# Performance work log

Hardware: AMD Instinct MI355X
Metric: run time of the kernel (lower is better)

Reference implementation:

```python
import jax, jax.numpy as jnp
import numpy as np

NPOINT = 1024
RADIUS = 0.2
NSAMPLE = 32


def furthest_point_sampling(xyz, npoint):
    # xyz: (B, N, 3) -> (B, npoint) int32 indices
    B, N, _ = xyz.shape

    def step(carry, _):
        dist, far = carry
        centroid = jnp.take_along_axis(xyz, far[:, None, None], axis=1)  # (B,1,3)
        d = jnp.sum((xyz - centroid) ** 2, axis=-1)                       # (B,N)
        dist = jnp.minimum(dist, d)
        new_far = jnp.argmax(dist, axis=-1).astype(jnp.int32)
        return (dist, new_far), far

    init = (jnp.full((B, N), 1e10, xyz.dtype), jnp.zeros((B,), jnp.int32))
    _, idx = jax.lax.scan(step, init, None, length=npoint)
    return idx.T  # (B, npoint)


def ball_query(xyz, new_xyz, radius, nsample):
    # xyz: (B,N,3), new_xyz: (B,S,3) -> (B,S,nsample) int32 indices
    N = xyz.shape[1]
    d2 = jnp.sum((new_xyz[:, :, None, :] - xyz[:, None, :, :]) ** 2, axis=-1)  # (B,S,N)
    # pick first `nsample` indices within radius (CUDA ball_query semantics)
    key = jnp.where(d2 < radius * radius, jnp.arange(N, dtype=jnp.int32)[None, None, :], N)
    idx = jnp.sort(key, axis=-1)[..., :nsample]          # (B,S,nsample)
    first = idx[..., :1]
    idx = jnp.where(idx == N, first, idx)                # pad with first valid
    return jnp.clip(idx, 0, N - 1).astype(jnp.int32)     # guard empty balls


def sa_forward(xyz, features, W1, s1, b1, W2, s2, b2, W3, s3, b3):
    B, N, _ = xyz.shape
    center_idx = furthest_point_sampling(xyz, NPOINT)                     # (B,S)
    new_xyz = jnp.take_along_axis(xyz, center_idx[..., None], axis=1)     # (B,S,3)

    idx = ball_query(xyz, new_xyz, RADIUS, NSAMPLE)                       # (B,S,K)
    # group xyz (relative coords) and features
    g_xyz = jnp.take_along_axis(xyz[:, None], idx[..., None], axis=2)     # (B,S,K,3)
    g_xyz = g_xyz - new_xyz[:, :, None, :]
    feats_n = jnp.swapaxes(features, 1, 2)                                # (B,N,C)
    g_feat = jnp.take_along_axis(feats_n[:, None], idx[..., None], axis=2)  # (B,S,K,C)
    g = jnp.concatenate([g_xyz, g_feat], axis=-1)                         # (B,S,K,3+C)
    x = jnp.transpose(g, (0, 3, 1, 2))                                    # (B,3+C,S,K)

    # 1x1 conv MLP with (folded) BN affine + ReLU
    for W, s, b in ((W1, s1, b1), (W2, s2, b2), (W3, s3, b3)):
        x = jax.nn.relu(jnp.einsum('oi,bisk->bosk', W, x)
                        * s[None, :, None, None] + b[None, :, None, None])
    new_features = jnp.max(x, axis=-1)                                    # (B,Cout,S)
    return new_xyz, new_features


def setup_inputs() -> dict:
    key = jax.random.key(0)
    ks = jax.random.split(key, 11)
    B, N, C = 4, 16384, 64
    return {
        'xyz': jax.random.uniform(ks[0], (B, N, 3), jnp.float32),
        'features': jax.random.normal(ks[1], (B, C, N), jnp.float32),
        'W1': jax.random.normal(ks[2], (64, C + 3), jnp.float32) * 0.1,
        's1': jax.random.uniform(ks[3], (64,), jnp.float32),
        'b1': jax.random.normal(ks[4], (64,), jnp.float32) * 0.1,
        'W2': jax.random.normal(ks[5], (64, 64), jnp.float32) * 0.1,
        's2': jax.random.uniform(ks[6], (64,), jnp.float32),
        'b2': jax.random.normal(ks[7], (64,), jnp.float32) * 0.1,
        'W3': jax.random.normal(ks[8], (128, 64), jnp.float32) * 0.1,
        's3': jax.random.uniform(ks[9], (128,), jnp.float32),
        'b3': jax.random.normal(ks[10], (128,), jnp.float32) * 0.1,
    }


def reference(xyz, features, W1, s1, b1, W2, s2, b2, W3, s3, b3):
    return sa_forward(xyz, features, W1, s1, b1, W2, s2, b2, W3, s3, b3)
```

## Files before the change

### kernel.cpp

```cpp
#include <hip/hip_runtime.h>
#include <cstdint>
#include <cstddef>

#define BATCH   4
#define NPTS    16384
#define NPOINT  1024
#define NSAMPLE 32
#define CIN     67
#define R2f     0.04f

#define FPS_T   512
#define FPS_P   32

template <int CTRL, int RMASK>
__device__ __forceinline__ void amax_dpp(float& v, int& i) {
  int nv = __builtin_amdgcn_update_dpp(__float_as_int(v), __float_as_int(v),
                                       CTRL, RMASK, 0xf, false);
  int ni = __builtin_amdgcn_update_dpp(i, i, CTRL, RMASK, 0xf, false);
  float fv = __int_as_float(nv);
  bool tk = (fv > v) || (fv == v && ni < i);
  v = tk ? fv : v;
  i = tk ? ni : i;
}

__global__ __launch_bounds__(FPS_T, 2) void fps_kernel(
    const float* __restrict__ xyz, float* __restrict__ out_newxyz)
{
  const int b = blockIdx.x;
  const float* base = xyz + (size_t)b * NPTS * 3;
  const int t = threadIdx.x;
  const int lane = t & 63, w = t >> 6;

  float px[FPS_P], py[FPS_P], pz[FPS_P], dist[FPS_P];
#pragma unroll
  for (int j = 0; j < FPS_P; ++j) {
    int p = t + (j << 9);
    px[j] = base[p * 3 + 0];
    py[j] = base[p * 3 + 1];
    pz[j] = base[p * 3 + 2];
    dist[j] = 1e10f;
  }

  __shared__ float s_wv[2][8];
  __shared__ int   s_wi[2][8];

  float cx = base[0], cy = base[1], cz = base[2];

  for (int it = 0; it < NPOINT; ++it) {
    if (t == 0) {
      int o = (b * NPOINT + it) * 3;
      out_newxyz[o + 0] = cx;
      out_newxyz[o + 1] = cy;
      out_newxyz[o + 2] = cz;
    }
    float bv = -1.0f; int bi = 0x7fffffff;
#pragma unroll
    for (int j = 0; j < FPS_P; ++j) {
      float dx = __fsub_rn(px[j], cx);
      float dy = __fsub_rn(py[j], cy);
      float dz = __fsub_rn(pz[j], cz);
      float d  = __fadd_rn(__fadd_rn(__fmul_rn(dx, dx), __fmul_rn(dy, dy)),
                           __fmul_rn(dz, dz));
      float nd = fminf(dist[j], d);
      dist[j] = nd;
      bool tk = nd > bv;
      bv = tk ? nd : bv;
      bi = tk ? (t + (j << 9)) : bi;
    }
    amax_dpp<0x121, 0xf>(bv, bi);
    amax_dpp<0x122, 0xf>(bv, bi);
    amax_dpp<0x124, 0xf>(bv, bi);
    amax_dpp<0x128, 0xf>(bv, bi);
    amax_dpp<0x142, 0xa>(bv, bi);
    amax_dpp<0x143, 0xc>(bv, bi);

    const int par = it & 1;
    if (lane == 63) { s_wv[par][w] = bv; s_wi[par][w] = bi; }
    __syncthreads();

    float gv = s_wv[par][lane & 7];
    int   gi = s_wi[par][lane & 7];
    amax_dpp<0x121, 0xf>(gv, gi);
    amax_dpp<0x122, 0xf>(gv, gi);
    amax_dpp<0x124, 0xf>(gv, gi);

    int far = __builtin_amdgcn_readfirstlane(gi);
    cx = base[far * 3 + 0];
    cy = base[far * 3 + 1];
    cz = base[far * 3 + 2];
  }
}

__global__ __launch_bounds__(256) void transpose_kernel(
    const float* __restrict__ f, float* __restrict__ ft)
{
  __shared__ float tile[64][65];
  int b  = blockIdx.x >> 8;
  int n0 = (blockIdx.x & 255) << 6;
  for (int v = threadIdx.x; v < 64 * 64; v += 256) {
    int c = v >> 6, j = v & 63;
    tile[c][j] = f[((size_t)(b * 64 + c)) * NPTS + n0 + j];
  }
  __syncthreads();
  for (int v = threadIdx.x; v < 64 * 64; v += 256) {
    int j = v >> 6, c = v & 63;
    ft[((size_t)(b * NPTS + n0 + j)) * 64 + c] = tile[c][j];
  }
}

__global__ __launch_bounds__(1024) void mlp_kernel(
    const float* __restrict__ xyz,
    const float* __restrict__ feats,
    const float* __restrict__ featsT,
    const float* __restrict__ nx,
    const float* __restrict__ W1, const float* __restrict__ s1, const float* __restrict__ b1,
    const float* __restrict__ W2, const float* __restrict__ s2, const float* __restrict__ b2,
    const float* __restrict__ W3, const float* __restrict__ s3, const float* __restrict__ b3,
    float* __restrict__ outF)
{
  __shared__ float W1t[CIN * 64];
  __shared__ float W2t[64 * 64];
  __shared__ float sb[512];
  __shared__ float xs[CIN * 34];
  __shared__ float h1[64 * 34];
  __shared__ float h2[64 * 34];
  __shared__ int   hm[128];
  __shared__ int   lid8[8][NSAMPLE];

  const int tid = threadIdx.x;
  const int lane = tid & 63, w = tid >> 6;

  for (int v = tid; v < CIN * 64; v += 1024) {
    int o = v / CIN, i = v - o * CIN;
    W1t[i * 64 + o] = W1[v];
  }
  for (int v = tid; v < 64 * 64; v += 1024) {
    int o = v >> 6, i = v & 63;
    W2t[i * 64 + o] = W2[v];
  }
  if (tid < 64)       sb[tid]       = s1[tid];
  else if (tid < 128) sb[tid]       = b1[tid - 64];
  else if (tid < 192) sb[tid]       = s2[tid - 128];
  else if (tid < 256) sb[tid]       = b2[tid - 192];
  else if (tid < 384) sb[tid]       = s3[tid - 256];
  else if (tid < 512) sb[tid]       = b3[tid - 384];

  if (w < 8) {
    int g = (blockIdx.x << 3) + w;
    int b = g >> 10;
    const float* base = xyz + (size_t)b * NPTS * 3;
    float cx = nx[g * 3 + 0], cy = nx[g * 3 + 1], cz = nx[g * 3 + 2];
    int cnt = 0, fidx = -1;
    for (int c0 = 0; c0 < NPTS && cnt < NSAMPLE; c0 += 64) {
      int i = c0 + lane;
      float dx = __fsub_rn(base[i * 3 + 0], cx);
      float dy = __fsub_rn(base[i * 3 + 1], cy);
      float dz = __fsub_rn(base[i * 3 + 2], cz);
      float d2 = __fadd_rn(__fadd_rn(__fmul_rn(dx, dx), __fmul_rn(dy, dy)),
                           __fmul_rn(dz, dz));
      bool pred = d2 < R2f;
      unsigned long long mk = __ballot(pred);
      if (pred) {
        int rank = cnt + __popcll(mk & ((1ull << lane) - 1ull));
        if (rank < NSAMPLE) lid8[w][rank] = i;
        if (rank == 0) fidx = i;
      }
      cnt += __popcll(mk);
    }
#pragma unroll
    for (int off = 32; off >= 1; off >>= 1) {
      int o = __shfl_xor(fidx, off);
      fidx = o > fidx ? o : fidx;
    }
    if (lane >= cnt && lane < NSAMPLE) lid8[w][lane] = fidx;
  }
  __syncthreads();

  for (int ci = 0; ci < 8; ++ci) {
    int g = (blockIdx.x << 3) + ci;
    int b = g >> 10, m = g & 1023;

    {
      int k = tid >> 5, c0 = tid & 31;
      int id = lid8[ci][k];
      for (int c = c0; c < CIN; c += 32) {
        float val;
        if (c < 3)
          val = __fsub_rn(xyz[((size_t)b * NPTS + id) * 3 + c], nx[g * 3 + c]);
        else if (featsT)
          val = featsT[((size_t)b * NPTS + id) * 64 + (c - 3)];
        else
          val = feats[((size_t)(b * 64 + (c - 3))) * NPTS + id];
        xs[c * 34 + k] = val;
      }
      if (tid < 128) hm[tid] = 0;
    }
    __syncthreads();

    {
      int oc = tid & 63, k0 = (tid >> 6) << 1;
      float a0 = 0.f, a1 = 0.f;
#pragma unroll 4
      for (int i = 0; i < CIN; ++i) {
        float ww = W1t[i * 64 + oc];
        a0 = fmaf(ww, xs[i * 34 + k0], a0);
        a1 = fmaf(ww, xs[i * 34 + k0 + 1], a1);
      }
      float s = sb[oc], bb = sb[64 + oc];
      h1[oc * 34 + k0]     = fmaxf(fmaf(a0, s, bb), 0.f);
      h1[oc * 34 + k0 + 1] = fmaxf(fmaf(a1, s, bb), 0.f);
    }
    __syncthreads();

    {
      int oc = tid & 63, k0 = (tid >> 6) << 1;
      float a0 = 0.f, a1 = 0.f;
#pragma unroll 4
      for (int i = 0; i < 64; ++i) {
        float ww = W2t[i * 64 + oc];
        a0 = fmaf(ww, h1[i * 34 + k0], a0);
        a1 = fmaf(ww, h1[i * 34 + k0 + 1], a1);
      }
      float s = sb[128 + oc], bb = sb[192 + oc];
      h2[oc * 34 + k0]     = fmaxf(fmaf(a0, s, bb), 0.f);
      h2[oc * 34 + k0 + 1] = fmaxf(fmaf(a1, s, bb), 0.f);
    }
    __syncthreads();

    {
      int oc = tid & 127, k0 = (tid >> 7) << 2;
      const float4* W3v = reinterpret_cast<const float4*>(W3);
      float a0 = 0.f, a1 = 0.f, a2 = 0.f, a3 = 0.f;
#pragma unroll 4
      for (int i4 = 0; i4 < 16; ++i4) {
        float4 wv = W3v[oc * 16 + i4];
        const float* hr = &h2[(i4 * 4) * 34 + k0];
        a0 = fmaf(wv.x, hr[0], a0); a1 = fmaf(wv.x, hr[1], a1);
        a2 = fmaf(wv.x, hr[2], a2); a3 = fmaf(wv.x, hr[3], a3);
        hr += 34;
        a0 = fmaf(wv.y, hr[0], a0); a1 = fmaf(wv.y, hr[1], a1);
        a2 = fmaf(wv.y, hr[2], a2); a3 = fmaf(wv.y, hr[3], a3);
        hr += 34;
        a0 = fmaf(wv.z, hr[0], a0); a1 = fmaf(wv.z, hr[1], a1);
        a2 = fmaf(wv.z, hr[2], a2); a3 = fmaf(wv.z, hr[3], a3);
        hr += 34;
        a0 = fmaf(wv.w, hr[0], a0); a1 = fmaf(wv.w, hr[1], a1);
        a2 = fmaf(wv.w, hr[2], a2); a3 = fmaf(wv.w, hr[3], a3);
      }
      float s = sb[256 + oc], bb = sb[384 + oc];
      float v0 = fmaxf(fmaf(a0, s, bb), 0.f);
      float v1 = fmaxf(fmaf(a1, s, bb), 0.f);
      float v2 = fmaxf(fmaf(a2, s, bb), 0.f);
      float v3 = fmaxf(fmaf(a3, s, bb), 0.f);
      float mv = fmaxf(fmaxf(v0, v1), fmaxf(v2, v3));
      atomicMax(&hm[oc], __float_as_int(mv));
    }
    __syncthreads();

    if (tid < 128)
      outF[(((size_t)b * 128 + tid) << 10) + m] = __int_as_float(hm[tid]);
    __syncthreads();
  }
}

extern "C" void kernel_launch(void* const* d_in, const int* in_sizes, int n_in,
                              void* d_out, int out_size, void* d_ws, size_t ws_size,
                              hipStream_t stream)
{
  if (n_in < 11) return;
  const float* xyz   = (const float*)d_in[0];
  const float* feats = (const float*)d_in[1];
  const float* W1 = (const float*)d_in[2];
  const float* s1 = (const float*)d_in[3];
  const float* b1 = (const float*)d_in[4];
  const float* W2 = (const float*)d_in[5];
  const float* s2 = (const float*)d_in[6];
  const float* b2 = (const float*)d_in[7];
  const float* W3 = (const float*)d_in[8];
  const float* s3 = (const float*)d_in[9];
  const float* b3 = (const float*)d_in[10];
  float* out = (float*)d_out;

  float* featsT = nullptr;
  size_t needT = (size_t)BATCH * NPTS * 64 * sizeof(float);
  if (ws_size >= needT) featsT = (float*)d_ws;

  fps_kernel<<<BATCH, FPS_T, 0, stream>>>(xyz, out);
  if (featsT) transpose_kernel<<<BATCH * 256, 256, 0, stream>>>(feats, featsT);
  mlp_kernel<<<512, 1024, 0, stream>>>(xyz, feats, featsT, out,
                                       W1, s1, b1, W2, s2, b2, W3, s3, b3,
                                       out + BATCH * NPOINT * 3);
}
```

Before: 2.255 ms.

## Widen FPS block to 1024 threads and use packed float2 distance math

Runs furthest point sampling with 1024 threads per batch instead of 512, so each thread holds 16 points rather than 32. The distance arithmetic now works on two-wide float vectors so it can map to packed FP32 instructions. The per-thread argmax records a local slot index and rebuilds the global index once per iteration. The cross-wave reduction grows to 16 waves and gains one extra DPP step. This targets the serial per-iteration latency of the FPS loop, at the cost of a larger barrier and reduction across more waves.

```diff
diff --git a/kernel.cpp b/kernel.cpp
--- a/kernel.cpp
+++ b/kernel.cpp
@@ -9,8 +9,12 @@
 #define CIN     67
 #define R2f     0.04f
 
-#define FPS_T   512
-#define FPS_P   32
+#define FPS_T   1024
+#define FPS_PRS 8
+
+typedef float v2f __attribute__((ext_vector_type(2)));
+
+#define RPT8(M) M(0)M(1)M(2)M(3)M(4)M(5)M(6)M(7)
 
 template <int CTRL, int RMASK>
 __device__ __forceinline__ void amax_dpp(float& v, int& i) {
@@ -23,7 +27,7 @@
   i = tk ? ni : i;
 }
 
-__global__ __launch_bounds__(FPS_T, 2) void fps_kernel(
+__global__ __launch_bounds__(FPS_T, 4) void fps_kernel(
     const float* __restrict__ xyz, float* __restrict__ out_newxyz)
 {
   const int b = blockIdx.x;
@@ -31,42 +35,45 @@
   const int t = threadIdx.x;
   const int lane = t & 63, w = t >> 6;
 
-  float px[FPS_P], py[FPS_P], pz[FPS_P], dist[FPS_P];
-#pragma unroll
-  for (int j = 0; j < FPS_P; ++j) {
-    int p = t + (j << 9);
-    px[j] = base[p * 3 + 0];
-    py[j] = base[p * 3 + 1];
-    pz[j] = base[p * 3 + 2];
-    dist[j] = 1e10f;
-  }
-
-  __shared__ float s_wv[2][8];
-  __shared__ int   s_wi[2][8];
-
-  float cx = base[0], cy = base[1], cz = base[2];
+#define DECLP(p) v2f xa##p, xb##p, zz##p; float da##p, db##p;
+  RPT8(DECLP)
+#undef DECLP
+#define LOADP(p) { const float* q0 = base + (size_t)(((2*(p)) << 10) + t) * 3; \
+                   const float* q1 = base + (size_t)(((2*(p)+1) << 10) + t) * 3; \
+                   xa##p.x = q0[0]; xa##p.y = q0[1]; \
+                   xb##p.x = q1[0]; xb##p.y = q1[1]; \
+                   zz##p.x = q0[2]; zz##p.y = q1[2]; \
+                   da##p = 1e10f;  db##p = 1e10f; }
+  RPT8(LOADP)
+#undef LOADP
+
+  __shared__ float s_wv[2][16];
+  __shared__ int   s_wi[2][16];
+
+  v2f cxy; cxy.x = base[0]; cxy.y = base[1];
+  v2f czz; czz.x = base[2]; czz.y = base[2];
 
   for (int it = 0; it < NPOINT; ++it) {
     if (t == 0) {
       int o = (b * NPOINT + it) * 3;
-      out_newxyz[o + 0] = cx;
-      out_newxyz[o + 1] = cy;
-      out_newxyz[o + 2] = cz;
-    }
-    float bv = -1.0f; int bi = 0x7fffffff;
-#pragma unroll
-    for (int j = 0; j < FPS_P; ++j) {
-      float dx = __fsub_rn(px[j], cx);
-      float dy = __fsub_rn(py[j], cy);
-      float dz = __fsub_rn(pz[j], cz);
-      float d  = __fadd_rn(__fadd_rn(__fmul_rn(dx, dx), __fmul_rn(dy, dy)),
-                           __fmul_rn(dz, dz));
-      float nd = fminf(dist[j], d);
-      dist[j] = nd;
-      bool tk = nd > bv;
-      bv = tk ? nd : bv;
-      bi = tk ? (t + (j << 9)) : bi;
-    }
+      out_newxyz[o + 0] = cxy.x;
+      out_newxyz[o + 1] = cxy.y;
+      out_newxyz[o + 2] = czz.x;
+    }
+    float bv = -1.0f; int bl = 0;
+#define STEPP(p) { \
+    v2f d0 = xa##p - cxy;  v2f d1 = xb##p - cxy;  v2f dz = zz##p - czz; \
+    v2f q0 = d0 * d0;      v2f q1 = d1 * d1;      v2f qz = dz * dz; \
+    float s0 = __fadd_rn(__fadd_rn(q0.x, q0.y), qz.x); \
+    float s1 = __fadd_rn(__fadd_rn(q1.x, q1.y), qz.y); \
+    float n0 = fminf(da##p, s0); da##p = n0; \
+    float n1 = fminf(db##p, s1); db##p = n1; \
+    bool t0 = n0 > bv; bv = t0 ? n0 : bv; bl = t0 ? (2*(p)) : bl; \
+    bool t1 = n1 > bv; bv = t1 ? n1 : bv; bl = t1 ? (2*(p)+1) : bl; }
+    RPT8(STEPP)
+#undef STEPP
+    int bi = (bl << 10) + t;
+
     amax_dpp<0x121, 0xf>(bv, bi);
     amax_dpp<0x122, 0xf>(bv, bi);
     amax_dpp<0x124, 0xf>(bv, bi);
@@ -78,16 +85,18 @@
     if (lane == 63) { s_wv[par][w] = bv; s_wi[par][w] = bi; }
     __syncthreads();
 
-    float gv = s_wv[par][lane & 7];
-    int   gi = s_wi[par][lane & 7];
+    float gv = s_wv[par][lane & 15];
+    int   gi = s_wi[par][lane & 15];
     amax_dpp<0x121, 0xf>(gv, gi);
     amax_dpp<0x122, 0xf>(gv, gi);
     amax_dpp<0x124, 0xf>(gv, gi);
+    amax_dpp<0x128, 0xf>(gv, gi);
 
     int far = __builtin_amdgcn_readfirstlane(gi);
-    cx = base[far * 3 + 0];
-    cy = base[far * 3 + 1];
-    cz = base[far * 3 + 2];
+    cxy.x = base[far * 3 + 0];
+    cxy.y = base[far * 3 + 1];
+    czz.x = base[far * 3 + 2];
+    czz.y = czz.x;
   }
 }
 
```

Result: slower. 2.440 ms (+8.2%).
